# Performance work log

Measured on AMD Instinct MI355X. Metric: run time of the kernel, lower is better.

## Reference

```python
import jax, jax.numpy as jnp
import numpy as np

B, S, E = 4, 4096, 128  # batch, seq_len, embedding_dim (quaternion groups)
D = 4 * E               # flattened feature dim fed to the Linear layers


def setup_inputs() -> dict:
    key = jax.random.key(0)
    ks = jax.random.split(key, 9)
    scale_w = 1.0 / np.sqrt(D).astype(np.float32)
    return {
        "query": jax.random.normal(ks[0], (B, S, E, 4), dtype=jnp.float32),
        "key": jax.random.normal(ks[1], (B, S, E, 4), dtype=jnp.float32),
        "value": jax.random.normal(ks[2], (B, S, E, 4), dtype=jnp.float32),
        "Wq": jax.random.normal(ks[3], (D, D), dtype=jnp.float32) * scale_w,
        "bq": jax.random.normal(ks[4], (D,), dtype=jnp.float32) * 0.01,
        "Wk": jax.random.normal(ks[5], (D, D), dtype=jnp.float32) * scale_w,
        "bk": jax.random.normal(ks[6], (D,), dtype=jnp.float32) * 0.01,
        "Wv": jax.random.normal(ks[7], (D, D), dtype=jnp.float32) * scale_w,
        "bv": jax.random.normal(ks[8], (D,), dtype=jnp.float32) * 0.01,
    }


def reference(query, key, value, Wq, bq, Wk, bk, Wv, bv):
    b, s = query.shape[0], query.shape[1]
    e = query.shape[2]  # embedding_dim
    # flatten quaternion dim: [B,S,E,4] -> [B,S,4E]
    q = query.reshape(b, s, -1)
    k = key.reshape(b, key.shape[1], -1)
    v = value.reshape(b, value.shape[1], -1)
    # torch nn.Linear: x @ W^T + bias
    Q = (q @ Wq.T + bq).reshape(b, s, -1, 4)
    K = (k @ Wk.T + bk).reshape(b, key.shape[1], -1, 4)
    V = (v @ Wv.T + bv).reshape(b, value.shape[1], -1, 4)
    # full QK^T over quaternion-grouped dims: [B,S,S]
    scores = jnp.einsum('bseq,bkeq->bsk', Q, K) / jnp.sqrt(jnp.float32(e))
    weights = jax.nn.softmax(scores, axis=-1)
    # faithful to the source: weights are summed over k and scale V at position s
    output = jnp.einsum('bsk,bseq->bseq', weights, V)
    return output, weights
```

## Files before the change

### kernel.cpp

```cpp
#include <hip/hip_runtime.h>
#include <cstdint>

typedef _Float16 h1;
typedef _Float16 h4 __attribute__((ext_vector_type(4)));
typedef _Float16 h8 __attribute__((ext_vector_type(8)));
typedef float    f4 __attribute__((ext_vector_type(4)));
typedef float    f32x4 __attribute__((ext_vector_type(4)));

#define NB 4
#define SL 4096
#define DD 512
#define MM (NB*SL)
#define SHIFT 12.0f

__global__ __launch_bounds__(256) void convert_w_kernel(
    const float* __restrict__ Wq, const float* __restrict__ Wk, const float* __restrict__ Wv,
    h1* __restrict__ Wh)
{
    const int per = DD*DD/4;
    int i = blockIdx.x * 256 + threadIdx.x;
    if (i >= 3*per) return;
    int mat = i / per;
    int j = i - mat*per;
    const float* src = (mat==0) ? Wq : (mat==1 ? Wk : Wv);
    f4 v = ((const f4*)src)[j];
    h4 hv;
    hv[0]=(h1)v[0]; hv[1]=(h1)v[1]; hv[2]=(h1)v[2]; hv[3]=(h1)v[3];
    ((h4*)(Wh + (size_t)mat*DD*DD))[j] = hv;
}

__global__ __launch_bounds__(256) void proj_gemm(
    const float* __restrict__ Xq, const float* __restrict__ Xk, const float* __restrict__ Xv,
    const h1* __restrict__ Wh,
    const float* __restrict__ bq, const float* __restrict__ bk, const float* __restrict__ bv,
    h1* __restrict__ Qh, h1* __restrict__ Kh, float* __restrict__ Vout)
{
    const int prj = blockIdx.z;
    const float* __restrict__ X    = (prj==0) ? Xq : (prj==1 ? Xk : Xv);
    const h1*    __restrict__ W    = Wh + (size_t)prj * DD * DD;
    const float* __restrict__ bias = (prj==0) ? bq : (prj==1 ? bk : bv);

    const int m0 = blockIdx.y * 128;
    const int n0 = blockIdx.x * 128;

    __shared__ h1 As[128][72];
    __shared__ h1 Bs[128][72];

    const int tid  = threadIdx.x;
    const int lane = tid & 63;
    const int wid  = tid >> 6;
    const int wm = wid >> 1, wn = wid & 1;
    const int g  = lane >> 4, c = lane & 15;
    const int r  = tid >> 1,  h = tid & 1;

    f32x4 acc[4][4];
    #pragma unroll
    for (int i = 0; i < 4; i++)
        #pragma unroll
        for (int j = 0; j < 4; j++) acc[i][j] = (f32x4){0.f, 0.f, 0.f, 0.f};

    for (int k0 = 0; k0 < DD; k0 += 64) {
        __syncthreads();
        {
            const f4* src = (const f4*)(X + (size_t)(m0 + r) * DD + k0 + h*32);
            f4 a0=src[0], a1=src[1], a2=src[2], a3=src[3],
               a4=src[4], a5=src[5], a6=src[6], a7=src[7];
            h8 p0, p1, p2, p3;
            #pragma unroll
            for (int j = 0; j < 4; j++) {
                p0[j]=(h1)a0[j]; p0[4+j]=(h1)a1[j];
                p1[j]=(h1)a2[j]; p1[4+j]=(h1)a3[j];
                p2[j]=(h1)a4[j]; p2[4+j]=(h1)a5[j];
                p3[j]=(h1)a6[j]; p3[4+j]=(h1)a7[j];
            }
            *(h8*)&As[r][h*32]      = p0;
            *(h8*)&As[r][h*32 + 8]  = p1;
            *(h8*)&As[r][h*32 + 16] = p2;
            *(h8*)&As[r][h*32 + 24] = p3;
        }
        {
            const h8* src = (const h8*)(W + (size_t)(n0 + r) * DD + k0 + h*32);
            h8 b0=src[0], b1=src[1], b2=src[2], b3=src[3];
            *(h8*)&Bs[r][h*32]      = b0;
            *(h8*)&Bs[r][h*32 + 8]  = b1;
            *(h8*)&Bs[r][h*32 + 16] = b2;
            *(h8*)&Bs[r][h*32 + 24] = b3;
        }
        __syncthreads();

        #pragma unroll
        for (int kk = 0; kk < 2; kk++) {
            h8 af[4], bf[4];
            #pragma unroll
            for (int mf = 0; mf < 4; mf++) af[mf] = *(const h8*)&As[wm*64 + mf*16 + c][kk*32 + g*8];
            #pragma unroll
            for (int nf = 0; nf < 4; nf++) bf[nf] = *(const h8*)&Bs[wn*64 + nf*16 + c][kk*32 + g*8];
            #pragma unroll
            for (int mf = 0; mf < 4; mf++)
                #pragma unroll
                for (int nf = 0; nf < 4; nf++)
                    acc[mf][nf] = __builtin_amdgcn_mfma_f32_16x16x32_f16(af[mf], bf[nf], acc[mf][nf], 0, 0, 0);
        }
    }

    float bv4[4];
    #pragma unroll
    for (int nf = 0; nf < 4; nf++) bv4[nf] = bias[n0 + wn*64 + nf*16 + c];

    #pragma unroll
    for (int mf = 0; mf < 4; mf++) {
        #pragma unroll
        for (int i = 0; i < 4; i++) {
            const int row = m0 + wm*64 + mf*16 + g*4 + i;
            #pragma unroll
            for (int nf = 0; nf < 4; nf++) {
                const int col = n0 + wn*64 + nf*16 + c;
                float vv = acc[mf][nf][i] + bv4[nf];
                if (prj == 0)      Qh[(size_t)row*DD + col] = (h1)vv;
                else if (prj == 1) Kh[(size_t)row*DD + col] = (h1)vv;
                else               Vout[(size_t)row*DD + col] = vv;
            }
        }
    }
}

__global__ __launch_bounds__(256) void scores_gemm(
    const h1* __restrict__ Qh, const h1* __restrict__ Kh,
    h1* __restrict__ Eh,
    float* __restrict__ partial)
{
    const int b  = blockIdx.z;
    const int m0 = blockIdx.y * 128;
    const int n0 = blockIdx.x * 128;
    const h1* __restrict__ Qb = Qh + (size_t)b * SL * DD;
    const h1* __restrict__ Kb = Kh + (size_t)b * SL * DD;

    __shared__ h1 As[128][72];
    __shared__ h1 Bs[128][72];

    const int tid  = threadIdx.x;
    const int lane = tid & 63;
    const int wid  = tid >> 6;
    const int wm = wid >> 1, wn = wid & 1;
    const int g  = lane >> 4, c = lane & 15;
    const int r  = tid >> 1,  h = tid & 1;

    f32x4 acc[4][4];
    #pragma unroll
    for (int i = 0; i < 4; i++)
        #pragma unroll
        for (int j = 0; j < 4; j++) acc[i][j] = (f32x4){0.f, 0.f, 0.f, 0.f};

    for (int k0 = 0; k0 < DD; k0 += 64) {
        __syncthreads();
        {
            const h8* sa = (const h8*)(Qb + (size_t)(m0 + r) * DD + k0 + h*32);
            h8 a0=sa[0], a1=sa[1], a2=sa[2], a3=sa[3];
            const h8* sb = (const h8*)(Kb + (size_t)(n0 + r) * DD + k0 + h*32);
            h8 b0=sb[0], b1=sb[1], b2=sb[2], b3=sb[3];
            *(h8*)&As[r][h*32]      = a0;
            *(h8*)&As[r][h*32 + 8]  = a1;
            *(h8*)&As[r][h*32 + 16] = a2;
            *(h8*)&As[r][h*32 + 24] = a3;
            *(h8*)&Bs[r][h*32]      = b0;
            *(h8*)&Bs[r][h*32 + 8]  = b1;
            *(h8*)&Bs[r][h*32 + 16] = b2;
            *(h8*)&Bs[r][h*32 + 24] = b3;
        }
        __syncthreads();

        #pragma unroll
        for (int kk = 0; kk < 2; kk++) {
            h8 af[4], bf[4];
            #pragma unroll
            for (int mf = 0; mf < 4; mf++) af[mf] = *(const h8*)&As[wm*64 + mf*16 + c][kk*32 + g*8];
            #pragma unroll
            for (int nf = 0; nf < 4; nf++) bf[nf] = *(const h8*)&Bs[wn*64 + nf*16 + c][kk*32 + g*8];
            #pragma unroll
            for (int mf = 0; mf < 4; mf++)
                #pragma unroll
                for (int nf = 0; nf < 4; nf++)
                    acc[mf][nf] = __builtin_amdgcn_mfma_f32_16x16x32_f16(af[mf], bf[nf], acc[mf][nf], 0, 0, 0);
        }
    }

    const float inv_scale = 0.08838834764831845f;
    #pragma unroll
    for (int mf = 0; mf < 4; mf++) {
        #pragma unroll
        for (int i = 0; i < 4; i++) {
            const int row = m0 + wm*64 + mf*16 + g*4 + i;
            h1* erow = Eh + ((size_t)b * SL + row) * SL;
            float rsum = 0.f;
            #pragma unroll
            for (int nf = 0; nf < 4; nf++) {
                const int col = n0 + wn*64 + nf*16 + c;
                float e = __expf(fmaf(acc[mf][nf][i], inv_scale, -SHIFT));
                erow[col] = (h1)e;
                rsum += e;
            }
            #pragma unroll
            for (int off = 1; off < 16; off <<= 1) rsum += __shfl_xor(rsum, off);
            if (c == 0)
                partial[((size_t)b * SL + row) * 64 + blockIdx.x * 2 + wn] = rsum;
        }
    }
}

__global__ __launch_bounds__(256) void rowsum_inv(
    const float* __restrict__ partial, float* __restrict__ invrow)
{
    int row = blockIdx.x * 256 + threadIdx.x;
    const f4* p = (const f4*)(partial + (size_t)row * 64);
    float s = 0.f;
    #pragma unroll
    for (int i = 0; i < 16; i++) { f4 v = p[i]; s += v[0] + v[1] + v[2] + v[3]; }
    invrow[row] = 1.0f / s;
}

__global__ __launch_bounds__(256) void normalize_k(
    const h1* __restrict__ Eh, const float* __restrict__ invrow,
    float* __restrict__ Wout)
{
    const size_t total8 = (size_t)NB * SL * SL / 8;
    size_t i = (size_t)blockIdx.x * blockDim.x + threadIdx.x;
    const size_t stride = (size_t)gridDim.x * blockDim.x;
    for (; i < total8; i += stride) {
        const int row = (int)(i >> 9);
        h8 v = ((const h8*)Eh)[i];
        const float s = invrow[row];
        f4 o0, o1;
        #pragma unroll
        for (int j = 0; j < 4; j++) { o0[j] = (float)v[j] * s; o1[j] = (float)v[4+j] * s; }
        ((f4*)Wout)[i*2]   = o0;
        ((f4*)Wout)[i*2+1] = o1;
    }
}

extern "C" void kernel_launch(void* const* d_in, const int* in_sizes, int n_in,
                              void* d_out, int out_size, void* d_ws, size_t ws_size,
                              hipStream_t stream)
{
    const float* q  = (const float*)d_in[0];
    const float* k  = (const float*)d_in[1];
    const float* v  = (const float*)d_in[2];
    const float* Wq = (const float*)d_in[3];
    const float* bq = (const float*)d_in[4];
    const float* Wk = (const float*)d_in[5];
    const float* bk = (const float*)d_in[6];
    const float* Wv = (const float*)d_in[7];
    const float* bv = (const float*)d_in[8];

    float* out  = (float*)d_out;
    float* Vout = out;
    float* Wout = out + (size_t)MM * DD;

    char* ws = (char*)d_ws;
    h1* Qh = (h1*)ws;
    h1* Kh = (h1*)(ws + (size_t)MM * DD * 2);
    h1* Wh = (h1*)(ws + (size_t)2 * MM * DD * 2);
    float* partial = (float*)(ws + (size_t)2*MM*DD*2 + (size_t)3*DD*DD*2);
    float* invrow  = (float*)((char*)partial + (size_t)MM * 64 * 4);
    h1* Eh = (h1*)((char*)invrow + (size_t)MM * 4);

    convert_w_kernel<<<768, 256, 0, stream>>>(Wq, Wk, Wv, Wh);
    proj_gemm<<<dim3(4, 128, 3), 256, 0, stream>>>(q, k, v, Wh, bq, bk, bv, Qh, Kh, Vout);
    scores_gemm<<<dim3(32, 32, NB), 256, 0, stream>>>(Qh, Kh, Eh, partial);
    rowsum_inv<<<MM / 256, 256, 0, stream>>>(partial, invrow);
    normalize_k<<<2048, 256, 0, stream>>>(Eh, invrow, Wout);
}
```

Measured before the change: 300.8 us.

## Stage GEMM tiles via direct global-to-LDS loads with swizzle; preconvert inputs to fp16

```diff
diff --git a/kernel.cpp b/kernel.cpp
--- a/kernel.cpp
+++ b/kernel.cpp
@@ -13,45 +13,78 @@
 #define MM (NB*SL)
 #define SHIFT 12.0f
 
-__global__ __launch_bounds__(256) void convert_w_kernel(
+__global__ __launch_bounds__(256) void convert_all(
+    const float* __restrict__ Xq, const float* __restrict__ Xk, const float* __restrict__ Xv,
     const float* __restrict__ Wq, const float* __restrict__ Wk, const float* __restrict__ Wv,
-    h1* __restrict__ Wh)
-{
-    const int per = DD*DD/4;
+    h1* __restrict__ Xh, h1* __restrict__ Wh)
+{
+    const int xper = MM*DD/4;
+    const int wper = DD*DD/4;
+    const int xtot = 3*xper;
     int i = blockIdx.x * 256 + threadIdx.x;
-    if (i >= 3*per) return;
-    int mat = i / per;
-    int j = i - mat*per;
-    const float* src = (mat==0) ? Wq : (mat==1 ? Wk : Wv);
+    const float* src;
+    h1* dst;
+    int j;
+    if (i < xtot) {
+        int mat = i / xper; j = i - mat*xper;
+        src = (mat==0) ? Xq : (mat==1 ? Xk : Xv);
+        dst = Xh + (size_t)mat*MM*DD;
+    } else {
+        int t = i - xtot;
+        if (t >= 3*wper) return;
+        int mat = t / wper; j = t - mat*wper;
+        src = (mat==0) ? Wq : (mat==1 ? Wk : Wv);
+        dst = Wh + (size_t)mat*DD*DD;
+    }
     f4 v = ((const f4*)src)[j];
     h4 hv;
     hv[0]=(h1)v[0]; hv[1]=(h1)v[1]; hv[2]=(h1)v[2]; hv[3]=(h1)v[3];
-    ((h4*)(Wh + (size_t)mat*DD*DD))[j] = hv;
+    ((h4*)dst)[j] = hv;
+}
+
+__device__ __forceinline__ void stage_tile(const h1* __restrict__ gbase,
+                                           h1* lds, int w, int l)
+{
+    #pragma unroll
+    for (int j = 0; j < 4; j++) {
+        const int cc  = w*4 + j;
+        const int row = cc*8 + (l >> 3);
+        const int sc  = (l & 7) ^ (l >> 3);
+        const h1* src = gbase + (size_t)row * DD + sc*8;
+        void* dst = (char*)lds + cc*1024;
+        __builtin_amdgcn_global_load_lds(
+            (const __attribute__((address_space(1))) uint32_t*)src,
+            (__attribute__((address_space(3))) uint32_t*)dst, 16, 0, 0);
+    }
+}
+
+__device__ __forceinline__ h8 lds_frag(const h1* lds, int row, int lc)
+{
+    const int chunk = lc ^ (row & 7);
+    return *(const h8*)(lds + row*64 + chunk*8);
 }
 
 __global__ __launch_bounds__(256) void proj_gemm(
-    const float* __restrict__ Xq, const float* __restrict__ Xk, const float* __restrict__ Xv,
-    const h1* __restrict__ Wh,
+    const h1* __restrict__ Xh, const h1* __restrict__ Wh,
     const float* __restrict__ bq, const float* __restrict__ bk, const float* __restrict__ bv,
     h1* __restrict__ Qh, h1* __restrict__ Kh, float* __restrict__ Vout)
 {
     const int prj = blockIdx.z;
-    const float* __restrict__ X    = (prj==0) ? Xq : (prj==1 ? Xk : Xv);
-    const h1*    __restrict__ W    = Wh + (size_t)prj * DD * DD;
+    const h1* __restrict__ X    = Xh + (size_t)prj * MM * DD;
+    const h1* __restrict__ W    = Wh + (size_t)prj * DD * DD;
     const float* __restrict__ bias = (prj==0) ? bq : (prj==1 ? bk : bv);
 
     const int m0 = blockIdx.y * 128;
     const int n0 = blockIdx.x * 128;
 
-    __shared__ h1 As[128][72];
-    __shared__ h1 Bs[128][72];
+    __shared__ h1 As[128*64];
+    __shared__ h1 Bs[128*64];
 
     const int tid  = threadIdx.x;
     const int lane = tid & 63;
     const int wid  = tid >> 6;
     const int wm = wid >> 1, wn = wid & 1;
     const int g  = lane >> 4, c = lane & 15;
-    const int r  = tid >> 1,  h = tid & 1;
 
     f32x4 acc[4][4];
     #pragma unroll
@@ -61,40 +94,16 @@
 
     for (int k0 = 0; k0 < DD; k0 += 64) {
         __syncthreads();
-        {
-            const f4* src = (const f4*)(X + (size_t)(m0 + r) * DD + k0 + h*32);
-            f4 a0=src[0], a1=src[1], a2=src[2], a3=src[3],
-               a4=src[4], a5=src[5], a6=src[6], a7=src[7];
-            h8 p0, p1, p2, p3;
-            #pragma unroll
-            for (int j = 0; j < 4; j++) {
-                p0[j]=(h1)a0[j]; p0[4+j]=(h1)a1[j];
-                p1[j]=(h1)a2[j]; p1[4+j]=(h1)a3[j];
-                p2[j]=(h1)a4[j]; p2[4+j]=(h1)a5[j];
-                p3[j]=(h1)a6[j]; p3[4+j]=(h1)a7[j];
-            }
-            *(h8*)&As[r][h*32]      = p0;
-            *(h8*)&As[r][h*32 + 8]  = p1;
-            *(h8*)&As[r][h*32 + 16] = p2;
-            *(h8*)&As[r][h*32 + 24] = p3;
-        }
-        {
-            const h8* src = (const h8*)(W + (size_t)(n0 + r) * DD + k0 + h*32);
-            h8 b0=src[0], b1=src[1], b2=src[2], b3=src[3];
-            *(h8*)&Bs[r][h*32]      = b0;
-            *(h8*)&Bs[r][h*32 + 8]  = b1;
-            *(h8*)&Bs[r][h*32 + 16] = b2;
-            *(h8*)&Bs[r][h*32 + 24] = b3;
-        }
-        __syncthreads();
-
+        stage_tile(X + (size_t)m0 * DD + k0, As, wid, lane);
+        stage_tile(W + (size_t)n0 * DD + k0, Bs, wid, lane);
+        __syncthreads();
         #pragma unroll
         for (int kk = 0; kk < 2; kk++) {
             h8 af[4], bf[4];
             #pragma unroll
-            for (int mf = 0; mf < 4; mf++) af[mf] = *(const h8*)&As[wm*64 + mf*16 + c][kk*32 + g*8];
-            #pragma unroll
-            for (int nf = 0; nf < 4; nf++) bf[nf] = *(const h8*)&Bs[wn*64 + nf*16 + c][kk*32 + g*8];
+            for (int mf = 0; mf < 4; mf++) af[mf] = lds_frag(As, wm*64 + mf*16 + c, kk*4 + g);
+            #pragma unroll
+            for (int nf = 0; nf < 4; nf++) bf[nf] = lds_frag(Bs, wn*64 + nf*16 + c, kk*4 + g);
             #pragma unroll
             for (int mf = 0; mf < 4; mf++)
                 #pragma unroll
@@ -135,15 +144,14 @@
     const h1* __restrict__ Qb = Qh + (size_t)b * SL * DD;
     const h1* __restrict__ Kb = Kh + (size_t)b * SL * DD;
 
-    __shared__ h1 As[128][72];
-    __shared__ h1 Bs[128][72];
+    __shared__ h1 As[128*64];
+    __shared__ h1 Bs[128*64];
 
     const int tid  = threadIdx.x;
     const int lane = tid & 63;
     const int wid  = tid >> 6;
     const int wm = wid >> 1, wn = wid & 1;
     const int g  = lane >> 4, c = lane & 15;
-    const int r  = tid >> 1,  h = tid & 1;
 
     f32x4 acc[4][4];
     #pragma unroll
@@ -153,29 +161,16 @@
 
     for (int k0 = 0; k0 < DD; k0 += 64) {
         __syncthreads();
-        {
-            const h8* sa = (const h8*)(Qb + (size_t)(m0 + r) * DD + k0 + h*32);
-            h8 a0=sa[0], a1=sa[1], a2=sa[2], a3=sa[3];
-            const h8* sb = (const h8*)(Kb + (size_t)(n0 + r) * DD + k0 + h*32);
-            h8 b0=sb[0], b1=sb[1], b2=sb[2], b3=sb[3];
-            *(h8*)&As[r][h*32]      = a0;
-            *(h8*)&As[r][h*32 + 8]  = a1;
-            *(h8*)&As[r][h*32 + 16] = a2;
-            *(h8*)&As[r][h*32 + 24] = a3;
-            *(h8*)&Bs[r][h*32]      = b0;
-            *(h8*)&Bs[r][h*32 + 8]  = b1;
-            *(h8*)&Bs[r][h*32 + 16] = b2;
-            *(h8*)&Bs[r][h*32 + 24] = b3;
-        }
-        __syncthreads();
-
+        stage_tile(Qb + (size_t)m0 * DD + k0, As, wid, lane);
+        stage_tile(Kb + (size_t)n0 * DD + k0, Bs, wid, lane);
+        __syncthreads();
         #pragma unroll
         for (int kk = 0; kk < 2; kk++) {
             h8 af[4], bf[4];
             #pragma unroll
-            for (int mf = 0; mf < 4; mf++) af[mf] = *(const h8*)&As[wm*64 + mf*16 + c][kk*32 + g*8];
-            #pragma unroll
-            for (int nf = 0; nf < 4; nf++) bf[nf] = *(const h8*)&Bs[wn*64 + nf*16 + c][kk*32 + g*8];
+            for (int mf = 0; mf < 4; mf++) af[mf] = lds_frag(As, wm*64 + mf*16 + c, kk*4 + g);
+            #pragma unroll
+            for (int nf = 0; nf < 4; nf++) bf[nf] = lds_frag(Bs, wn*64 + nf*16 + c, kk*4 + g);
             #pragma unroll
             for (int mf = 0; mf < 4; mf++)
                 #pragma unroll
@@ -256,15 +251,17 @@
     float* Wout = out + (size_t)MM * DD;
 
     char* ws = (char*)d_ws;
-    h1* Qh = (h1*)ws;
-    h1* Kh = (h1*)(ws + (size_t)MM * DD * 2);
-    h1* Wh = (h1*)(ws + (size_t)2 * MM * DD * 2);
-    float* partial = (float*)(ws + (size_t)2*MM*DD*2 + (size_t)3*DD*DD*2);
-    float* invrow  = (float*)((char*)partial + (size_t)MM * 64 * 4);
-    h1* Eh = (h1*)((char*)invrow + (size_t)MM * 4);
-
-    convert_w_kernel<<<768, 256, 0, stream>>>(Wq, Wk, Wv, Wh);
-    proj_gemm<<<dim3(4, 128, 3), 256, 0, stream>>>(q, k, v, Wh, bq, bk, bv, Qh, Kh, Vout);
+    h1* Xh = (h1*)ws;
+    h1* Wh = (h1*)(ws + (size_t)3*MM*DD*2);
+    h1* Qh = (h1*)((char*)Wh + (size_t)3*DD*DD*2);
+    h1* Kh = (h1*)((char*)Qh + (size_t)MM*DD*2);
+    float* partial = (float*)((char*)Kh + (size_t)MM*DD*2);
+    float* invrow  = (float*)((char*)partial + (size_t)MM*64*4);
+    h1* Eh = (h1*)((char*)invrow + (size_t)MM*4);
+
+    const int conv_chunks = (3*MM*DD + 3*DD*DD) / 4;
+    convert_all<<<(conv_chunks + 255)/256, 256, 0, stream>>>(q, k, v, Wq, Wk, Wv, Xh, Wh);
+    proj_gemm<<<dim3(4, 128, 3), 256, 0, stream>>>(Xh, Wh, bq, bk, bv, Qh, Kh, Vout);
     scores_gemm<<<dim3(32, 32, NB), 256, 0, stream>>>(Qh, Kh, Eh, partial);
     rowsum_inv<<<MM / 256, 256, 0, stream>>>(partial, invrow);
     normalize_k<<<2048, 256, 0, stream>>>(Eh, invrow, Wout);
```

New measurement: 296.7 us. About the same (-1.4%).

## Stage GEMM fp16 tiles via direct global-to-LDS loads with XOR swizzle

Applied to the files above, without the earlier changes.

```diff
diff --git a/kernel.cpp b/kernel.cpp
--- a/kernel.cpp
+++ b/kernel.cpp
@@ -29,6 +29,28 @@
     ((h4*)(Wh + (size_t)mat*DD*DD))[j] = hv;
 }
 
+__device__ __forceinline__ void stage_tile(const h1* __restrict__ gbase,
+                                           h1* lds, int w, int l)
+{
+    #pragma unroll
+    for (int j = 0; j < 4; j++) {
+        const int cc  = w*4 + j;
+        const int row = cc*8 + (l >> 3);
+        const int sc  = (l & 7) ^ (l >> 3);
+        const h1* src = gbase + (size_t)row * DD + sc*8;
+        void* dst = (char*)lds + cc*1024;
+        __builtin_amdgcn_global_load_lds(
+            (const __attribute__((address_space(1))) uint32_t*)src,
+            (__attribute__((address_space(3))) uint32_t*)dst, 16, 0, 0);
+    }
+}
+
+__device__ __forceinline__ h8 lds_frag(const h1* lds, int row, int lc)
+{
+    const int chunk = lc ^ (row & 7);
+    return *(const h8*)(lds + row*64 + chunk*8);
+}
+
 __global__ __launch_bounds__(256) void proj_gemm(
     const float* __restrict__ Xq, const float* __restrict__ Xk, const float* __restrict__ Xv,
     const h1* __restrict__ Wh,
@@ -44,7 +66,7 @@
     const int n0 = blockIdx.x * 128;
 
     __shared__ h1 As[128][72];
-    __shared__ h1 Bs[128][72];
+    __shared__ h1 Bs[128*64];
 
     const int tid  = threadIdx.x;
     const int lane = tid & 63;
@@ -61,6 +83,7 @@
 
     for (int k0 = 0; k0 < DD; k0 += 64) {
         __syncthreads();
+        stage_tile(W + (size_t)n0 * DD + k0, Bs, wid, lane);
         {
             const f4* src = (const f4*)(X + (size_t)(m0 + r) * DD + k0 + h*32);
             f4 a0=src[0], a1=src[1], a2=src[2], a3=src[3],
@@ -78,14 +101,6 @@
             *(h8*)&As[r][h*32 + 16] = p2;
             *(h8*)&As[r][h*32 + 24] = p3;
         }
-        {
-            const h8* src = (const h8*)(W + (size_t)(n0 + r) * DD + k0 + h*32);
-            h8 b0=src[0], b1=src[1], b2=src[2], b3=src[3];
-            *(h8*)&Bs[r][h*32]      = b0;
-            *(h8*)&Bs[r][h*32 + 8]  = b1;
-            *(h8*)&Bs[r][h*32 + 16] = b2;
-            *(h8*)&Bs[r][h*32 + 24] = b3;
-        }
         __syncthreads();
 
         #pragma unroll
@@ -94,7 +109,7 @@
             #pragma unroll
             for (int mf = 0; mf < 4; mf++) af[mf] = *(const h8*)&As[wm*64 + mf*16 + c][kk*32 + g*8];
             #pragma unroll
-            for (int nf = 0; nf < 4; nf++) bf[nf] = *(const h8*)&Bs[wn*64 + nf*16 + c][kk*32 + g*8];
+            for (int nf = 0; nf < 4; nf++) bf[nf] = lds_frag(Bs, wn*64 + nf*16 + c, kk*4 + g);
             #pragma unroll
             for (int mf = 0; mf < 4; mf++)
                 #pragma unroll
@@ -135,15 +150,14 @@
     const h1* __restrict__ Qb = Qh + (size_t)b * SL * DD;
     const h1* __restrict__ Kb = Kh + (size_t)b * SL * DD;
 
-    __shared__ h1 As[128][72];
-    __shared__ h1 Bs[128][72];
+    __shared__ h1 As[128*64];
+    __shared__ h1 Bs[128*64];
 
     const int tid  = threadIdx.x;
     const int lane = tid & 63;
     const int wid  = tid >> 6;
     const int wm = wid >> 1, wn = wid & 1;
     const int g  = lane >> 4, c = lane & 15;
-    const int r  = tid >> 1,  h = tid & 1;
 
     f32x4 acc[4][4];
     #pragma unroll
@@ -153,29 +167,16 @@
 
     for (int k0 = 0; k0 < DD; k0 += 64) {
         __syncthreads();
-        {
-            const h8* sa = (const h8*)(Qb + (size_t)(m0 + r) * DD + k0 + h*32);
-            h8 a0=sa[0], a1=sa[1], a2=sa[2], a3=sa[3];
-            const h8* sb = (const h8*)(Kb + (size_t)(n0 + r) * DD + k0 + h*32);
-            h8 b0=sb[0], b1=sb[1], b2=sb[2], b3=sb[3];
-            *(h8*)&As[r][h*32]      = a0;
-            *(h8*)&As[r][h*32 + 8]  = a1;
-            *(h8*)&As[r][h*32 + 16] = a2;
-            *(h8*)&As[r][h*32 + 24] = a3;
-            *(h8*)&Bs[r][h*32]      = b0;
-            *(h8*)&Bs[r][h*32 + 8]  = b1;
-            *(h8*)&Bs[r][h*32 + 16] = b2;
-            *(h8*)&Bs[r][h*32 + 24] = b3;
-        }
-        __syncthreads();
-
+        stage_tile(Qb + (size_t)m0 * DD + k0, As, wid, lane);
+        stage_tile(Kb + (size_t)n0 * DD + k0, Bs, wid, lane);
+        __syncthreads();
         #pragma unroll
         for (int kk = 0; kk < 2; kk++) {
             h8 af[4], bf[4];
             #pragma unroll
-            for (int mf = 0; mf < 4; mf++) af[mf] = *(const h8*)&As[wm*64 + mf*16 + c][kk*32 + g*8];
-            #pragma unroll
-            for (int nf = 0; nf < 4; nf++) bf[nf] = *(const h8*)&Bs[wn*64 + nf*16 + c][kk*32 + g*8];
+            for (int mf = 0; mf < 4; mf++) af[mf] = lds_frag(As, wm*64 + mf*16 + c, kk*4 + g);
+            #pragma unroll
+            for (int nf = 0; nf < 4; nf++) bf[nf] = lds_frag(Bs, wn*64 + nf*16 + c, kk*4 + g);
             #pragma unroll
             for (int mf = 0; mf < 4; mf++)
                 #pragma unroll
@@ -232,8 +233,8 @@
         f4 o0, o1;
         #pragma unroll
         for (int j = 0; j < 4; j++) { o0[j] = (float)v[j] * s; o1[j] = (float)v[4+j] * s; }
-        ((f4*)Wout)[i*2]   = o0;
-        ((f4*)Wout)[i*2+1] = o1;
+        __builtin_nontemporal_store(o0, ((f4*)Wout) + i*2);
+        __builtin_nontemporal_store(o1, ((f4*)Wout) + i*2 + 1);
     }
 }
 
@@ -256,16 +257,16 @@
     float* Wout = out + (size_t)MM * DD;
 
     char* ws = (char*)d_ws;
-    h1* Qh = (h1*)ws;
-    h1* Kh = (h1*)(ws + (size_t)MM * DD * 2);
-    h1* Wh = (h1*)(ws + (size_t)2 * MM * DD * 2);
-    float* partial = (float*)(ws + (size_t)2*MM*DD*2 + (size_t)3*DD*DD*2);
-    float* invrow  = (float*)((char*)partial + (size_t)MM * 64 * 4);
-    h1* Eh = (h1*)((char*)invrow + (size_t)MM * 4);
+    h1* Wh = (h1*)ws;
+    h1* Qh = (h1*)(ws + (size_t)3*DD*DD*2);
+    h1* Kh = (h1*)((char*)Qh + (size_t)MM*DD*2);
+    float* partial = (float*)((char*)Kh + (size_t)MM*DD*2);
+    float* invrow  = (float*)((char*)partial + (size_t)MM*64*4);
+    h1* Eh = (h1*)((char*)invrow + (size_t)MM*4);
 
     convert_w_kernel<<<768, 256, 0, stream>>>(Wq, Wk, Wv, Wh);
     proj_gemm<<<dim3(4, 128, 3), 256, 0, stream>>>(q, k, v, Wh, bq, bk, bv, Qh, Kh, Vout);
     scores_gemm<<<dim3(32, 32, NB), 256, 0, stream>>>(Qh, Kh, Eh, partial);
     rowsum_inv<<<MM / 256, 256, 0, stream>>>(partial, invrow);
-    normalize_k<<<2048, 256, 0, stream>>>(Eh, invrow, Wout);
-}
+    normalize_k<<<4096, 256, 0, stream>>>(Eh, invrow, Wout);
+}
```

New measurement: 310.9 us. 3.3% more time.
